# Kernel tuning notes

Hardware: AMD Instinct MI355X
Metric: run time of the kernel (lower is better)

Reference implementation:

```python
import jax, jax.numpy as jnp
import numpy as np

IN_F = 256
OUT_F = 256
BOND_F = 6
EPS = 1e-5


def setup_inputs() -> dict:
    key = jax.random.key(0)
    ks = jax.random.split(key, 24)
    n_atoms, n_bonds = 200000, 260000
    counts = {1: 20000, 2: 60000, 3: 60000, 4: 40000, 5: 20000}
    inp = {}
    inp["atom_features"] = jax.random.normal(ks[0], (n_atoms, IN_F), jnp.float32)
    inp["bond_features"] = jax.random.normal(ks[1], (n_bonds, BOND_F), jnp.float32)
    i = 2
    for d, n in counts.items():
        inp[f"atom_nbrs_{d}"] = jax.random.randint(ks[i], (n, d), 0, n_atoms); i += 1
        inp[f"bond_nbrs_{d}"] = jax.random.randint(ks[i], (n, d), 0, n_bonds); i += 1
    # parameters (Linear stored as [in, out] so y = x @ W)
    inp["W_self"] = jax.random.normal(ks[i], (IN_F, OUT_F), jnp.float32) * 0.05; i += 1
    inp["bias"] = jnp.zeros((OUT_F,), jnp.float32)
    for d in counts:
        inp[f"W_deg_{d}"] = jax.random.normal(ks[i], (IN_F + BOND_F, OUT_F), jnp.float32) * 0.05; i += 1
    inp["bn_weight"] = jnp.ones((OUT_F,), jnp.float32)
    inp["bn_bias"] = jnp.zeros((OUT_F,), jnp.float32)
    return inp


def reference(atom_features, bond_features,
              atom_nbrs_1, atom_nbrs_2, atom_nbrs_3, atom_nbrs_4, atom_nbrs_5,
              bond_nbrs_1, bond_nbrs_2, bond_nbrs_3, bond_nbrs_4, bond_nbrs_5,
              W_self, bias, W_deg_1, W_deg_2, W_deg_3, W_deg_4, W_deg_5,
              bn_weight, bn_bias):
    self_act = atom_features @ W_self  # [N, out]
    atom_nbrs = (atom_nbrs_1, atom_nbrs_2, atom_nbrs_3, atom_nbrs_4, atom_nbrs_5)
    bond_nbrs = (bond_nbrs_1, bond_nbrs_2, bond_nbrs_3, bond_nbrs_4, bond_nbrs_5)
    W_degs = (W_deg_1, W_deg_2, W_deg_3, W_deg_4, W_deg_5)
    acts = []
    for an, bn, W in zip(atom_nbrs, bond_nbrs, W_degs):
        # gather [n_d, deg, F], sum over neighbors, concat atom+bond feats
        summed = jnp.concatenate(
            [atom_features[an].sum(axis=1), bond_features[bn].sum(axis=1)], axis=-1)
        acts.append(summed @ W)  # [n_d, out]
    neighbour_act = jnp.concatenate(acts, axis=0)  # [N, out] (atoms ordered by degree)
    total = jax.nn.relu(neighbour_act + self_act + bias)
    # BatchNorm1d (training mode: batch stats, biased variance)
    mean = total.mean(axis=0)
    var = jnp.mean((total - mean) ** 2, axis=0)
    return (total - mean) / jnp.sqrt(var + EPS) * bn_weight + bn_bias
```

## Files before the change

kernel.cpp:

```cpp
#include <hip/hip_runtime.h>

typedef __bf16 bf16;
typedef bf16 bf16x4_t __attribute__((ext_vector_type(4)));
typedef bf16 bf16x8_t __attribute__((ext_vector_type(8)));
typedef float f32x4_t __attribute__((ext_vector_type(4)));

#define IN_F   256
#define OUT_F  256
#define BOND_F 6
#define KTOT   544
#define KCH    17
#define XSTRIDE 552

__global__ void pack_w_kernel(const float* __restrict__ Ws,
                              const float* __restrict__ W1, const float* __restrict__ W2,
                              const float* __restrict__ W3, const float* __restrict__ W4,
                              const float* __restrict__ W5, bf16* __restrict__ Wpk)
{
    int idx = blockIdx.x * 256 + threadIdx.x;
    if (idx >= 5 * KTOT * 256) return;
    int deg  = idx / (KTOT * 256);
    int rem  = idx - deg * (KTOT * 256);
    int kq   = rem >> 11;
    int rem2 = rem & 2047;
    int n    = rem2 >> 3;
    int j    = rem2 & 7;
    int k    = kq * 8 + j;
    const float* Wd = (deg == 0) ? W1 : (deg == 1) ? W2 : (deg == 2) ? W3
                                      : (deg == 3) ? W4 : W5;
    float v = 0.f;
    if (k < 256)      v = Ws[k * 256 + n];
    else if (k < 518) v = Wd[(k - 256) * 256 + n];
    Wpk[idx] = (bf16)v;
}

template<int D>
__global__ __launch_bounds__(256, 2)
void gemm_deg(const float* __restrict__ atomF, const float* __restrict__ bondF,
              const int* __restrict__ an, const int* __restrict__ bnb,
              const bf16* __restrict__ Wpk, const float* __restrict__ bias,
              float* __restrict__ out, float* __restrict__ accum,
              int n_d, int row_off)
{
    __shared__ bf16 Xs[64][XSTRIDE];

    const int tid  = threadIdx.x;
    const int q    = tid >> 6;
    const int c    = tid & 63;
    const int blk0 = blockIdx.x * 64;

    for (int it = 0; it < 16; ++it) {
        const int r  = it * 4 + q;
        const int rl = blk0 + r;
        const int rc = (rl < n_d) ? rl : (n_d - 1);

        const float4 sv = *(const float4*)(atomF + (size_t)(row_off + rc) * IN_F + c * 4);
        float4 nv = make_float4(0.f, 0.f, 0.f, 0.f);
        #pragma unroll
        for (int j = 0; j < D; ++j) {
            const int idx = an[rc * D + j];
            const float4 v = *(const float4*)(atomF + (size_t)idx * IN_F + c * 4);
            nv.x += v.x; nv.y += v.y; nv.z += v.z; nv.w += v.w;
        }
        bf16x4_t s4 = { (bf16)sv.x, (bf16)sv.y, (bf16)sv.z, (bf16)sv.w };
        bf16x4_t n4 = { (bf16)nv.x, (bf16)nv.y, (bf16)nv.z, (bf16)nv.w };
        *(bf16x4_t*)&Xs[r][c * 4]       = s4;
        *(bf16x4_t*)&Xs[r][256 + c * 4] = n4;
    }
    if (tid < 64) {
        const int r  = tid;
        const int rl = blk0 + r;
        const int rc = (rl < n_d) ? rl : (n_d - 1);
        float b[BOND_F] = {0.f, 0.f, 0.f, 0.f, 0.f, 0.f};
        #pragma unroll
        for (int j = 0; j < D; ++j) {
            const float* bp = bondF + (size_t)bnb[rc * D + j] * BOND_F;
            const float2 b0 = *(const float2*)(bp + 0);
            const float2 b1 = *(const float2*)(bp + 2);
            const float2 b2 = *(const float2*)(bp + 4);
            b[0] += b0.x; b[1] += b0.y; b[2] += b1.x;
            b[3] += b1.y; b[4] += b2.x; b[5] += b2.y;
        }
        #pragma unroll
        for (int t = 0; t < BOND_F; ++t) Xs[r][512 + t] = (bf16)b[t];
        #pragma unroll
        for (int t = 518; t < KTOT; ++t) Xs[r][t] = (bf16)0.f;
    }
    __syncthreads();

    const int w    = q;
    const int lane = tid & 63;
    const int l15  = lane & 15;
    const int quad = lane >> 4;

    f32x4_t acc[4][4] = {};

    for (int kc = 0; kc < KCH; ++kc) {
        bf16x8_t a[4], b[4];
        #pragma unroll
        for (int rt = 0; rt < 4; ++rt)
            a[rt] = *(const bf16x8_t*)&Xs[rt * 16 + l15][kc * 32 + quad * 8];
        #pragma unroll
        for (int ct = 0; ct < 4; ++ct) {
            const int n = w * 64 + ct * 16 + l15;
            b[ct] = *(const bf16x8_t*)(Wpk + ((size_t)((kc * 4 + quad) * 256 + n) << 3));
        }
        #pragma unroll
        for (int rt = 0; rt < 4; ++rt)
            #pragma unroll
            for (int ct = 0; ct < 4; ++ct)
                acc[rt][ct] = __builtin_amdgcn_mfma_f32_16x16x32_bf16(
                    a[rt], b[ct], acc[rt][ct], 0, 0, 0);
    }

    float csum[4] = {0.f, 0.f, 0.f, 0.f};
    float csq[4]  = {0.f, 0.f, 0.f, 0.f};
    #pragma unroll
    for (int ct = 0; ct < 4; ++ct) {
        const int n = w * 64 + ct * 16 + l15;
        const float bs = bias[n];
        #pragma unroll
        for (int rt = 0; rt < 4; ++rt) {
            #pragma unroll
            for (int rg = 0; rg < 4; ++rg) {
                const int m  = rt * 16 + quad * 4 + rg;
                const int rl = blk0 + m;
                if (rl < n_d) {
                    float v = acc[rt][ct][rg] + bs;
                    v = fmaxf(v, 0.f);
                    out[(size_t)(row_off + rl) * OUT_F + n] = v;
                    csum[ct] += v;
                    csq[ct]  += v * v;
                }
            }
        }
    }
    #pragma unroll
    for (int ct = 0; ct < 4; ++ct) {
        float s  = csum[ct];
        float sq = csq[ct];
        s  += __shfl_xor(s, 16, 64);  s  += __shfl_xor(s, 32, 64);
        sq += __shfl_xor(sq, 16, 64); sq += __shfl_xor(sq, 32, 64);
        if (quad == 0) {
            const int n = w * 64 + ct * 16 + l15;
            atomicAdd(accum + n, s);
            atomicAdd(accum + 256 + n, sq);
        }
    }
}

__global__ void bn_finalize(const float* __restrict__ accum,
                            const float* __restrict__ bnw, const float* __restrict__ bnb,
                            float* __restrict__ ss, int n_rows)
{
    const int t = threadIdx.x;
    const float inv_n = 1.f / (float)n_rows;
    const float mean  = accum[t] * inv_n;
    const float var   = accum[256 + t] * inv_n - mean * mean;
    const float inv   = rsqrtf(var + 1e-5f);
    const float sc    = bnw[t] * inv;
    ss[t]       = sc;
    ss[256 + t] = bnb[t] - mean * sc;
}

__global__ __launch_bounds__(256)
void bn_apply(float* __restrict__ out, const float* __restrict__ ss, size_t n4)
{
    __shared__ float4 s4[64], h4[64];
    if (threadIdx.x < 64) {
        s4[threadIdx.x] = ((const float4*)ss)[threadIdx.x];
        h4[threadIdx.x] = ((const float4*)(ss + 256))[threadIdx.x];
    }
    __syncthreads();
    const size_t stride = (size_t)gridDim.x * blockDim.x;
    for (size_t i = (size_t)blockIdx.x * blockDim.x + threadIdx.x; i < n4; i += stride) {
        float4 v = ((float4*)out)[i];
        const int c = (int)(i & 63);
        const float4 s = s4[c];
        const float4 h = h4[c];
        v.x = v.x * s.x + h.x;
        v.y = v.y * s.y + h.y;
        v.z = v.z * s.z + h.z;
        v.w = v.w * s.w + h.w;
        ((float4*)out)[i] = v;
    }
}

extern "C" void kernel_launch(void* const* d_in, const int* in_sizes, int n_in,
                              void* d_out, int out_size, void* d_ws, size_t ws_size,
                              hipStream_t stream)
{
    const float* atomF = (const float*)d_in[0];
    const float* bondF = (const float*)d_in[1];
    const int* an[5];
    const int* bnp[5];
    int n_d[5];
    for (int d = 0; d < 5; ++d) {
        an[d]  = (const int*)d_in[2 + 2 * d];
        bnp[d] = (const int*)d_in[3 + 2 * d];
        n_d[d] = in_sizes[2 + 2 * d] / (d + 1);
    }
    const float* Wself = (const float*)d_in[12];
    const float* bias  = (const float*)d_in[13];
    const float* Wd[5] = {(const float*)d_in[14], (const float*)d_in[15],
                          (const float*)d_in[16], (const float*)d_in[17],
                          (const float*)d_in[18]};
    const float* bnw = (const float*)d_in[19];
    const float* bnb = (const float*)d_in[20];
    float* out = (float*)d_out;

    char* ws = (char*)d_ws;
    bf16*  Wpk   = (bf16*)ws;
    float* accum = (float*)(ws + 1392640);
    float* ss    = (float*)(ws + 1394688);

    int n_atoms = in_sizes[0] / IN_F;

    hipMemsetAsync(accum, 0, 512 * sizeof(float), stream);

    pack_w_kernel<<<(5 * KTOT * 256 + 255) / 256, 256, 0, stream>>>(
        Wself, Wd[0], Wd[1], Wd[2], Wd[3], Wd[4], Wpk);

    int row_off = 0;
    {
        int g = (n_d[0] + 63) / 64;
        gemm_deg<1><<<g, 256, 0, stream>>>(atomF, bondF, an[0], bnp[0],
            Wpk + 0 * KTOT * 256, bias, out, accum, n_d[0], row_off);
        row_off += n_d[0];
    }
    {
        int g = (n_d[1] + 63) / 64;
        gemm_deg<2><<<g, 256, 0, stream>>>(atomF, bondF, an[1], bnp[1],
            Wpk + 1 * KTOT * 256, bias, out, accum, n_d[1], row_off);
        row_off += n_d[1];
    }
    {
        int g = (n_d[2] + 63) / 64;
        gemm_deg<3><<<g, 256, 0, stream>>>(atomF, bondF, an[2], bnp[2],
            Wpk + 2 * KTOT * 256, bias, out, accum, n_d[2], row_off);
        row_off += n_d[2];
    }
    {
        int g = (n_d[3] + 63) / 64;
        gemm_deg<4><<<g, 256, 0, stream>>>(atomF, bondF, an[3], bnp[3],
            Wpk + 3 * KTOT * 256, bias, out, accum, n_d[3], row_off);
        row_off += n_d[3];
    }
    {
        int g = (n_d[4] + 63) / 64;
        gemm_deg<5><<<g, 256, 0, stream>>>(atomF, bondF, an[4], bnp[4],
            Wpk + 4 * KTOT * 256, bias, out, accum, n_d[4], row_off);
        row_off += n_d[4];
    }

    bn_finalize<<<1, 256, 0, stream>>>(accum, bnw, bnb, ss, n_atoms);

    size_t n4 = (size_t)out_size / 4;
    bn_apply<<<8192, 256, 0, stream>>>(out, ss, n4);
}
```

Measured before the change: 721.1 us.

## Pre-cast atom features to bf16 and merge degree GEMMs into one launch

Adds a kernel that converts atom features to bf16 once, so the neighbour gathers read half as many bytes with 16-byte vector loads. The five per-degree launches are merged into a single grid with segment lookup, scheduled with the highest degree first to reduce tail idle time. Neighbour indices are prefetched into registers before the gather loop. In exchange it adds an extra full pass over the atom features for the cast, extra workspace, and summation of bf16-rounded inputs.

Result: faster. 638.0 us (-11.5%).

```diff
diff --git a/kernel.cpp b/kernel.cpp
--- a/kernel.cpp
+++ b/kernel.cpp
@@ -11,6 +11,27 @@
 #define KTOT   544
 #define KCH    17
 #define XSTRIDE 552
+
+struct SegArgs {
+    const int* an[5];
+    const int* bnb[5];
+    const bf16* W[5];
+    int n_d[5];
+    int row_off[5];
+    int blk_end[5];
+};
+
+__global__ __launch_bounds__(256)
+void cast_atoms(const float* __restrict__ in, bf16* __restrict__ out, int n8)
+{
+    int i = blockIdx.x * 256 + threadIdx.x;
+    if (i >= n8) return;
+    const float4 a = ((const float4*)in)[2 * i];
+    const float4 b = ((const float4*)in)[2 * i + 1];
+    bf16x8_t o = { (bf16)a.x, (bf16)a.y, (bf16)a.z, (bf16)a.w,
+                   (bf16)b.x, (bf16)b.y, (bf16)b.z, (bf16)b.w };
+    ((bf16x8_t*)out)[i] = o;
+}
 
 __global__ void pack_w_kernel(const float* __restrict__ Ws,
                               const float* __restrict__ W1, const float* __restrict__ W2,
@@ -35,37 +56,47 @@
 }
 
 template<int D>
-__global__ __launch_bounds__(256, 2)
-void gemm_deg(const float* __restrict__ atomF, const float* __restrict__ bondF,
-              const int* __restrict__ an, const int* __restrict__ bnb,
-              const bf16* __restrict__ Wpk, const float* __restrict__ bias,
-              float* __restrict__ out, float* __restrict__ accum,
-              int n_d, int row_off)
-{
-    __shared__ bf16 Xs[64][XSTRIDE];
-
+__device__ __forceinline__
+void gemm_body(const bf16* __restrict__ atomB, const float* __restrict__ bondF,
+               const int* __restrict__ an, const int* __restrict__ bnb,
+               const bf16* __restrict__ Wpk, const float* __restrict__ bias,
+               float* __restrict__ out, float* __restrict__ accum,
+               int n_d, int row_off, int blk_local, bf16 (*Xs)[XSTRIDE])
+{
     const int tid  = threadIdx.x;
-    const int q    = tid >> 6;
-    const int c    = tid & 63;
-    const int blk0 = blockIdx.x * 64;
-
-    for (int it = 0; it < 16; ++it) {
-        const int r  = it * 4 + q;
-        const int rl = blk0 + r;
-        const int rc = (rl < n_d) ? rl : (n_d - 1);
-
-        const float4 sv = *(const float4*)(atomF + (size_t)(row_off + rc) * IN_F + c * 4);
-        float4 nv = make_float4(0.f, 0.f, 0.f, 0.f);
-        #pragma unroll
-        for (int j = 0; j < D; ++j) {
-            const int idx = an[rc * D + j];
-            const float4 v = *(const float4*)(atomF + (size_t)idx * IN_F + c * 4);
-            nv.x += v.x; nv.y += v.y; nv.z += v.z; nv.w += v.w;
-        }
-        bf16x4_t s4 = { (bf16)sv.x, (bf16)sv.y, (bf16)sv.z, (bf16)sv.w };
-        bf16x4_t n4 = { (bf16)nv.x, (bf16)nv.y, (bf16)nv.z, (bf16)nv.w };
-        *(bf16x4_t*)&Xs[r][c * 4]       = s4;
-        *(bf16x4_t*)&Xs[r][256 + c * 4] = n4;
+    const int blk0 = blk_local * 64;
+
+    {
+        const int rg = tid >> 5;
+        const int c  = tid & 31;
+
+        int idxs[8][D];
+        #pragma unroll
+        for (int it = 0; it < 8; ++it) {
+            const int rl = blk0 + it * 8 + rg;
+            const int rc = (rl < n_d) ? rl : (n_d - 1);
+            #pragma unroll
+            for (int j = 0; j < D; ++j) idxs[it][j] = an[rc * D + j];
+        }
+
+        for (int it = 0; it < 8; ++it) {
+            const int r  = it * 8 + rg;
+            const int rl = blk0 + r;
+            const int rc = (rl < n_d) ? rl : (n_d - 1);
+            const bf16x8_t sv = *(const bf16x8_t*)(atomB + (size_t)(row_off + rc) * IN_F + c * 8);
+            float nv[8] = {0.f, 0.f, 0.f, 0.f, 0.f, 0.f, 0.f, 0.f};
+            #pragma unroll
+            for (int j = 0; j < D; ++j) {
+                const bf16x8_t v = *(const bf16x8_t*)(atomB + (size_t)idxs[it][j] * IN_F + c * 8);
+                #pragma unroll
+                for (int t = 0; t < 8; ++t) nv[t] += (float)v[t];
+            }
+            bf16x8_t n8;
+            #pragma unroll
+            for (int t = 0; t < 8; ++t) n8[t] = (bf16)nv[t];
+            *(bf16x8_t*)&Xs[r][c * 8]       = sv;
+            *(bf16x8_t*)&Xs[r][256 + c * 8] = n8;
+        }
     }
     if (tid < 64) {
         const int r  = tid;
@@ -88,7 +119,7 @@
     }
     __syncthreads();
 
-    const int w    = q;
+    const int w    = tid >> 6;
     const int lane = tid & 63;
     const int l15  = lane & 15;
     const int quad = lane >> 4;
@@ -146,6 +177,34 @@
             atomicAdd(accum + n, s);
             atomicAdd(accum + 256 + n, sq);
         }
+    }
+}
+
+__global__ __launch_bounds__(256, 2)
+void gemm_all(SegArgs S, const bf16* __restrict__ atomB, const float* __restrict__ bondF,
+              const float* __restrict__ bias, float* __restrict__ out,
+              float* __restrict__ accum)
+{
+    __shared__ bf16 Xs[64][XSTRIDE];
+    const int b = blockIdx.x;
+    int s;
+    if      (b < S.blk_end[0]) s = 0;
+    else if (b < S.blk_end[1]) s = 1;
+    else if (b < S.blk_end[2]) s = 2;
+    else if (b < S.blk_end[3]) s = 3;
+    else                       s = 4;
+    const int bl = b - ((s == 0) ? 0 : S.blk_end[s - 1]);
+    switch (s) {
+    case 0: gemm_body<5>(atomB, bondF, S.an[0], S.bnb[0], S.W[0], bias, out, accum,
+                         S.n_d[0], S.row_off[0], bl, Xs); break;
+    case 1: gemm_body<4>(atomB, bondF, S.an[1], S.bnb[1], S.W[1], bias, out, accum,
+                         S.n_d[1], S.row_off[1], bl, Xs); break;
+    case 2: gemm_body<3>(atomB, bondF, S.an[2], S.bnb[2], S.W[2], bias, out, accum,
+                         S.n_d[2], S.row_off[2], bl, Xs); break;
+    case 3: gemm_body<2>(atomB, bondF, S.an[3], S.bnb[3], S.W[3], bias, out, accum,
+                         S.n_d[3], S.row_off[3], bl, Xs); break;
+    default: gemm_body<1>(atomB, bondF, S.an[4], S.bnb[4], S.W[4], bias, out, accum,
+                          S.n_d[4], S.row_off[4], bl, Xs); break;
     }
 }
 
@@ -213,45 +272,36 @@
     bf16*  Wpk   = (bf16*)ws;
     float* accum = (float*)(ws + 1392640);
     float* ss    = (float*)(ws + 1394688);
-
-    int n_atoms = in_sizes[0] / IN_F;
+    bf16*  atomB = (bf16*)(ws + 1396736);
+
+    const int n_atoms = in_sizes[0] / IN_F;
 
     hipMemsetAsync(accum, 0, 512 * sizeof(float), stream);
+
+    const int n8 = n_atoms * IN_F / 8;
+    cast_atoms<<<(n8 + 255) / 256, 256, 0, stream>>>(atomF, atomB, n8);
 
     pack_w_kernel<<<(5 * KTOT * 256 + 255) / 256, 256, 0, stream>>>(
         Wself, Wd[0], Wd[1], Wd[2], Wd[3], Wd[4], Wpk);
 
-    int row_off = 0;
-    {
-        int g = (n_d[0] + 63) / 64;
-        gemm_deg<1><<<g, 256, 0, stream>>>(atomF, bondF, an[0], bnp[0],
-            Wpk + 0 * KTOT * 256, bias, out, accum, n_d[0], row_off);
-        row_off += n_d[0];
-    }
-    {
-        int g = (n_d[1] + 63) / 64;
-        gemm_deg<2><<<g, 256, 0, stream>>>(atomF, bondF, an[1], bnp[1],
-            Wpk + 1 * KTOT * 256, bias, out, accum, n_d[1], row_off);
-        row_off += n_d[1];
-    }
-    {
-        int g = (n_d[2] + 63) / 64;
-        gemm_deg<3><<<g, 256, 0, stream>>>(atomF, bondF, an[2], bnp[2],
-            Wpk + 2 * KTOT * 256, bias, out, accum, n_d[2], row_off);
-        row_off += n_d[2];
-    }
-    {
-        int g = (n_d[3] + 63) / 64;
-        gemm_deg<4><<<g, 256, 0, stream>>>(atomF, bondF, an[3], bnp[3],
-            Wpk + 3 * KTOT * 256, bias, out, accum, n_d[3], row_off);
-        row_off += n_d[3];
-    }
-    {
-        int g = (n_d[4] + 63) / 64;
-        gemm_deg<5><<<g, 256, 0, stream>>>(atomF, bondF, an[4], bnp[4],
-            Wpk + 4 * KTOT * 256, bias, out, accum, n_d[4], row_off);
-        row_off += n_d[4];
-    }
+    int row_off_d[5];
+    int ro = 0;
+    for (int d = 0; d < 5; ++d) { row_off_d[d] = ro; ro += n_d[d]; }
+
+    SegArgs S;
+    int cum = 0;
+    for (int s = 0; s < 5; ++s) {
+        const int d = 4 - s;
+        S.an[s]      = an[d];
+        S.bnb[s]     = bnp[d];
+        S.W[s]       = Wpk + (size_t)d * KTOT * 256;
+        S.n_d[s]     = n_d[d];
+        S.row_off[s] = row_off_d[d];
+        cum += (n_d[d] + 63) / 64;
+        S.blk_end[s] = cum;
+    }
+
+    gemm_all<<<cum, 256, 0, stream>>>(S, atomB, bondF, bias, out, accum);
 
     bn_finalize<<<1, 256, 0, stream>>>(accum, bnw, bnb, ss, n_atoms);
 
```
